# Kernel tuning notes

Measured on AMD Instinct MI355X. Metric: run time of the kernel, lower is better.

Reference implementation:

```python
import jax, jax.numpy as jnp
import numpy as np

B, S, E, H, L, OUT = 128, 256, 300, 512, 2, 2


def _lstm_dir(x, mask, w_ih, w_hh, b, h0, c0, reverse):
    """One direction of one LSTM layer with length masking (packed-seq semantics).
    x: [B,S,D], mask: [B,S] bool (t < length). Returns (outputs [B,S,H], final h [B,H]).
    For reverse=True, scan runs t=S-1..0; state only updates once t < length, which
    exactly reproduces pack_padded_sequence reverse-direction behavior.
    """
    def step(carry, inp):
        h, c = carry
        xt, mt = inp  # [B,D], [B]
        z = xt @ w_ih.T + h @ w_hh.T + b  # [B,4H], torch gate order i,f,g,o
        i, f, g, o = jnp.split(z, 4, axis=-1)
        c_new = jax.nn.sigmoid(f) * c + jax.nn.sigmoid(i) * jnp.tanh(g)
        h_new = jax.nn.sigmoid(o) * jnp.tanh(c_new)
        m = mt[:, None]
        h = jnp.where(m, h_new, h)
        c = jnp.where(m, c_new, c)
        return (h, c), h
    (hT, _), hs = jax.lax.scan(step, (h0, c0), (jnp.swapaxes(x, 0, 1), mask.T), reverse=reverse)
    return jnp.swapaxes(hs, 0, 1), hT


def setup_inputs():
    key = jax.random.key(0)
    ks = iter(jax.random.split(key, 32))
    lengths = jax.random.randint(next(ks), (B,), 1, S + 1)
    x = jax.random.normal(next(ks), (B, S, E), jnp.float32)
    # module encodes per-sample lengths in input[:, -1, 0]
    x = x.at[:, -1, 0].set(lengths.astype(jnp.float32))
    k = 1.0 / np.sqrt(H)
    def u(shape):
        return jax.random.uniform(next(ks), shape, jnp.float32, -k, k)
    d = {"x": x}
    for l in range(L):
        din = E if l == 0 else 2 * H
        for suf in ("f", "r"):
            d[f"w_ih_l{l}_{suf}"] = u((4 * H, din))
            d[f"w_hh_l{l}_{suf}"] = u((4 * H, H))
            d[f"b_ih_l{l}_{suf}"] = u((4 * H,))
            d[f"b_hh_l{l}_{suf}"] = u((4 * H,))
    d["fc1_w"] = u((H, H))
    d["fc1_b"] = u((H,))
    d["fc_w"] = u((OUT, H))
    d["fc_b"] = u((OUT,))
    return d


def _forward(x, params):
    Bx, Sx = x.shape[0], x.shape[1]
    lengths = jnp.minimum(x[:, -1, 0].astype(jnp.int32), Sx)  # clamp(max=seq_len)
    mask = jnp.arange(Sx)[None, :] < lengths[:, None]  # [B,S]
    h0 = jnp.ones((Bx, H), x.dtype)  # module uses ones, not zeros
    c0 = jnp.ones((Bx, H), x.dtype)
    inp = x
    hT_r = None
    for l in range(L):
        (wif, whf, bif, bhf), (wir, whr, bir, bhr) = params[l]
        out_f, _ = _lstm_dir(inp, mask, wif, whf, bif + bhf, h0, c0, False)
        out_r, hT_r = _lstm_dir(inp, mask, wir, whr, bir + bhr, h0, c0, True)
        inp = jnp.concatenate([out_f, out_r], axis=-1)  # [B,S,2H]
    # ht[-1] == final hidden of reverse direction of last layer
    return hT_r


def reference(x, w_ih_l0_f, w_hh_l0_f, b_ih_l0_f, b_hh_l0_f,
              w_ih_l0_r, w_hh_l0_r, b_ih_l0_r, b_hh_l0_r,
              w_ih_l1_f, w_hh_l1_f, b_ih_l1_f, b_hh_l1_f,
              w_ih_l1_r, w_hh_l1_r, b_ih_l1_r, b_hh_l1_r,
              fc1_w, fc1_b, fc_w, fc_b):
    params = [((w_ih_l0_f, w_hh_l0_f, b_ih_l0_f, b_hh_l0_f),
               (w_ih_l0_r, w_hh_l0_r, b_ih_l0_r, b_hh_l0_r)),
              ((w_ih_l1_f, w_hh_l1_f, b_ih_l1_f, b_hh_l1_f),
               (w_ih_l1_r, w_hh_l1_r, b_ih_l1_r, b_hh_l1_r))]
    ht = _forward(x, params)  # [B,H]
    out = ht @ fc1_w.T + fc1_b  # fc1 (no activation in original)
    return out @ fc_w.T + fc_b  # [B,OUT]
```

## Files before the change

### kernel.cpp

```cpp
#include <hip/hip_runtime.h>

#define B_  128
#define S_  256
#define E_  300
#define EP_ 320
#define H_  512
#define G_  2048
#define D1_ 1024

typedef _Float16 f16;
typedef __attribute__((ext_vector_type(8))) _Float16 f16x8;
typedef __attribute__((ext_vector_type(4))) float    f32x4;
typedef unsigned long long u64;
typedef unsigned int u32;

__device__ __forceinline__ float sigf(float x){ return 1.f/(1.f + __expf(-x)); }
__device__ __forceinline__ float tanhf_(float x){
  float e = __expf(-2.f*fabsf(x));
  float t = (1.f - e)/(1.f + e);
  return x < 0.f ? -t : t;
}

__device__ __forceinline__ u64 aload64(const u64* p){
  return __hip_atomic_load((u64*)p, __ATOMIC_RELAXED, __HIP_MEMORY_SCOPE_AGENT);
}
__device__ __forceinline__ void astore32(u32* p, u32 v){
  __hip_atomic_store(p, v, __ATOMIC_RELAXED, __HIP_MEMORY_SCOPE_AGENT);
}
union H8 { u64 q[2]; f16x8 v; };
union FU { f16 f; unsigned short s; };


__global__ void k_f32_to_f16(const float* __restrict__ s, f16* __restrict__ d, int n){
  int i = blockIdx.x*blockDim.x + threadIdx.x;
  if (i < n) d[i] = (f16)s[i];
}

__global__ void k_pad_w(const float* __restrict__ s, f16* __restrict__ d, int rows, int ks, int kd){
  int i = blockIdx.x*blockDim.x + threadIdx.x;
  if (i >= rows*kd) return;
  int r = i/kd, k = i - r*kd;
  d[i] = (k < ks) ? (f16)s[(size_t)r*ks + k] : (f16)0.f;
}

__global__ void k_bias(const float* __restrict__ a, const float* __restrict__ b,
                       float* __restrict__ d, int n){
  int i = blockIdx.x*blockDim.x + threadIdx.x;
  if (i < n) d[i] = a[i] + b[i];
}

__global__ void k_len(const float* __restrict__ x, int* __restrict__ len){
  int b = threadIdx.x;
  if (b < B_){
    int v = (int)x[((size_t)b*S_ + (S_-1))*E_];
    len[b] = v > S_ ? S_ : v;
  }
}

__global__ void k_init(f16* hxA, f16* hx1, float* cstate, u32* barA, u32* barC){
  int i = blockIdx.x*blockDim.x + threadIdx.x;
  if (i < B_*H_){
    hxA[i] = (f16)1.f;
    hxA[2*B_*H_ + i] = (f16)1.f;
    hx1[i] = (f16)1.f;
    cstate[i] = 1.f;
  }
  if (i < 4*S_) barA[i] = 0u;
  if (i < 2*S_) barC[i] = 0u;
}


__global__ __launch_bounds__(256) void k_gemm_bt(
    const f16* __restrict__ A, const f16* __restrict__ Bm,
    f16* __restrict__ C, const float* __restrict__ bias,
    int M, int N, int K)
{
  __shared__ f16 As[64*40];
  __shared__ f16 Bs[64*40];
  const int m0 = blockIdx.x*64, n0 = blockIdx.y*64;
  const int tid = threadIdx.x;
  const int w = tid>>6, lane = tid&63, quad = lane>>4, l16 = lane&15;
  const int wm = (w&1)*32, wn = (w>>1)*32;
  const int lr = tid>>2, lc = (tid&3)*8;
  const f16* Ap = A + (size_t)(m0+lr)*K + lc;
  const f16* Bp = Bm + (size_t)(n0+lr)*K + lc;
  f32x4 z4 = {0.f,0.f,0.f,0.f};
  f32x4 acc[2][2] = {{z4,z4},{z4,z4}};
  for (int k0 = 0; k0 < K; k0 += 32){
    *(uint4*)&As[lr*40+lc] = *(const uint4*)(Ap + k0);
    *(uint4*)&Bs[lr*40+lc] = *(const uint4*)(Bp + k0);
    __syncthreads();
    f16x8 a0 = *(const f16x8*)&As[(wm+l16)*40 + quad*8];
    f16x8 a1 = *(const f16x8*)&As[(wm+16+l16)*40 + quad*8];
    f16x8 b0 = *(const f16x8*)&Bs[(wn+l16)*40 + quad*8];
    f16x8 b1 = *(const f16x8*)&Bs[(wn+16+l16)*40 + quad*8];
    acc[0][0] = __builtin_amdgcn_mfma_f32_16x16x32_f16(a0,b0,acc[0][0],0,0,0);
    acc[0][1] = __builtin_amdgcn_mfma_f32_16x16x32_f16(a0,b1,acc[0][1],0,0,0);
    acc[1][0] = __builtin_amdgcn_mfma_f32_16x16x32_f16(a1,b0,acc[1][0],0,0,0);
    acc[1][1] = __builtin_amdgcn_mfma_f32_16x16x32_f16(a1,b1,acc[1][1],0,0,0);
    __syncthreads();
  }
#pragma unroll
  for (int mi = 0; mi < 2; ++mi)
#pragma unroll
    for (int ni = 0; ni < 2; ++ni){
      int col = n0 + wn + ni*16 + l16;
      float bz = bias[col];
#pragma unroll
      for (int r = 0; r < 4; ++r){
        int row = m0 + wm + mi*16 + quad*4 + r;
        C[(size_t)row*N + col] = (f16)(acc[mi][ni][r] + bz);
      }
    }
}


__global__ __launch_bounds__(256, 1) void k_phaseA(
    const float* __restrict__ x,
    const f16* __restrict__ w0f, const f16* __restrict__ w0r,
    const f16* __restrict__ whf, const f16* __restrict__ whr,
    const float* __restrict__ bs0, const int* __restrict__ len,
    f16* __restrict__ hxA, f16* __restrict__ outcat,
    u32* __restrict__ barA)
{
  __shared__ f16 Wh[64*512];
  __shared__ f16 Wi[64*320];
  const int half = blockIdx.x, jb = blockIdx.y, dir = blockIdx.z;
  const f16* wih = dir ? w0r : w0f;
  const f16* whh = dir ? whr : whf;
  const float* bias = bs0 + dir*G_;
  f16* hx = hxA + (size_t)dir*(2*B_*H_);
  u32* mybar = barA + (dir*2 + half)*S_;
  const int tid = threadIdx.x;
  const int w = tid>>6, lane = tid&63, quad = lane>>4, l16 = lane&15;
  const int j0 = jb*16;
  const int m0 = half*64 + w*16;

  for (int u = tid; u < 4096; u += 256){
    int lrr = u>>6, uc = u&63;
    int g = lrr>>4, i = lrr&15;
    *(uint4*)&Wh[lrr*512 + (uc ^ (i&7))*8] =
        *(const uint4*)(whh + ((size_t)(g*H_ + j0 + i))*H_ + uc*8);
  }
  for (int u = tid; u < 2560; u += 256){
    int row = u/40, c = u - row*40;
    int g = row>>4, i = row&15;
    *(uint4*)&Wi[row*320 + (c ^ (i&7))*8] =
        *(const uint4*)(wih + ((size_t)(g*H_ + j0 + i))*EP_ + c*8);
  }
  __syncthreads();

  const int j = j0 + l16;
  float bz[4], hprev[4], cpr[4]; int lm[4];
#pragma unroll
  for (int g = 0; g < 4; ++g) bz[g] = bias[g*H_ + j];
#pragma unroll
  for (int r = 0; r < 4; ++r){ hprev[r] = 1.f; cpr[r] = 1.f; lm[r] = len[m0 + quad*4 + r]; }
  const size_t xrowbase = (size_t)(m0 + l16)*S_;

  float4 xA[9], xB[9]; float xT[8];
  {
    const int t0 = dir ? (S_-1) : 0;
    const float* xr = x + (xrowbase + t0)*E_;
#pragma unroll
    for (int kb = 0; kb < 9; ++kb){
      xA[kb] = *(const float4*)(xr + kb*32 + quad*8);
      xB[kb] = *(const float4*)(xr + kb*32 + quad*8 + 4);
    }
    int kbase = 288 + quad*8;
#pragma unroll
    for (int e2 = 0; e2 < 8; ++e2)
      xT[e2] = (kbase + e2 < E_) ? xr[kbase + e2] : 0.f;
  }

  for (int s = 0; s < S_; ++s){
    const int t = dir ? (S_-1-s) : s;
    f32x4 z4 = {0.f,0.f,0.f,0.f};
    f32x4 acc[4] = {z4,z4,z4,z4};

#pragma unroll
    for (int kb = 0; kb < 9; ++kb){
      f16x8 a;
      a[0]=(f16)xA[kb].x; a[1]=(f16)xA[kb].y; a[2]=(f16)xA[kb].z; a[3]=(f16)xA[kb].w;
      a[4]=(f16)xB[kb].x; a[5]=(f16)xB[kb].y; a[6]=(f16)xB[kb].z; a[7]=(f16)xB[kb].w;
      int c = (kb*4 + quad) ^ (l16 & 7);
#pragma unroll
      for (int g = 0; g < 4; ++g){
        f16x8 b = *(const f16x8*)&Wi[(g*16+l16)*320 + c*8];
        acc[g] = __builtin_amdgcn_mfma_f32_16x16x32_f16(a, b, acc[g],0,0,0);
      }
    }
    {
      f16x8 a;
#pragma unroll
      for (int e2 = 0; e2 < 8; ++e2) a[e2] = (f16)xT[e2];
      int c = (36 + quad) ^ (l16 & 7);
#pragma unroll
      for (int g = 0; g < 4; ++g){
        f16x8 b = *(const f16x8*)&Wi[(g*16+l16)*320 + c*8];
        acc[g] = __builtin_amdgcn_mfma_f32_16x16x32_f16(a, b, acc[g],0,0,0);
      }
    }

    if (s+1 < S_){
      const int tn = dir ? (S_-2-s) : (s+1);
      const float* xr = x + (xrowbase + tn)*E_;
#pragma unroll
      for (int kb = 0; kb < 9; ++kb){
        xA[kb] = *(const float4*)(xr + kb*32 + quad*8);
        xB[kb] = *(const float4*)(xr + kb*32 + quad*8 + 4);
      }
      int kbase = 288 + quad*8;
#pragma unroll
      for (int e2 = 0; e2 < 8; ++e2)
        xT[e2] = (kbase + e2 < E_) ? xr[kbase + e2] : 0.f;
    }

    if (s > 0){
      while (__hip_atomic_load(&mybar[s-1], __ATOMIC_RELAXED, __HIP_MEMORY_SCOPE_AGENT) < 32u) {}
    }
    asm volatile("" ::: "memory");

    const int par = s & 1;
    const u64* hap = (const u64*)(hx + (size_t)par*(B_*H_) + (size_t)(m0 + l16)*H_);
    u64 hq[32];
#pragma unroll
    for (int kb = 0; kb < 16; ++kb){
      hq[2*kb]   = aload64(hap + kb*8 + quad*2);
      hq[2*kb+1] = aload64(hap + kb*8 + quad*2 + 1);
    }
#pragma unroll
    for (int kb = 0; kb < 16; ++kb){
      H8 ha;
      ha.q[0] = hq[2*kb];
      ha.q[1] = hq[2*kb+1];
      int uq = kb*4 + quad;
#pragma unroll
      for (int g = 0; g < 4; ++g){
        f16x8 b = *(const f16x8*)&Wh[(g*16+l16)*512 + ((uq ^ (l16&7)))*8];
        acc[g] = __builtin_amdgcn_mfma_f32_16x16x32_f16(ha.v, b, acc[g],0,0,0);
      }
    }

    f16* hn = hx + (size_t)(1-par)*(B_*H_);
#pragma unroll
    for (int r = 0; r < 4; ++r){
      int m = m0 + quad*4 + r;
      float zi = acc[0][r] + bz[0];
      float zf = acc[1][r] + bz[1];
      float zg = acc[2][r] + bz[2];
      float zo = acc[3][r] + bz[3];
      float ig = sigf(zi), fg = sigf(zf), gg = tanhf_(zg), og = sigf(zo);
      float cnew = fg*cpr[r] + ig*gg;
      float hnew = og*tanhf_(cnew);
      bool mk = t < lm[r];
      float hsel = mk ? hnew : hprev[r];
      cpr[r] = mk ? cnew : cpr[r];
      hprev[r] = hsel;
      FU cv; cv.f = (f16)hsel;
      int other = __shfl_down((int)cv.s, 1);
      if ((l16 & 1) == 0)
        astore32((u32*)(hn + (size_t)m*H_ + j), (u32)cv.s | ((u32)other << 16));
    }
    __syncthreads();
    if (tid == 0)
      __hip_atomic_fetch_add(&mybar[s], 1u, __ATOMIC_RELAXED, __HIP_MEMORY_SCOPE_AGENT);

#pragma unroll
    for (int r = 0; r < 4; ++r){
      int m = m0 + quad*4 + r;
      FU cv; cv.f = (f16)hprev[r];
      int other = __shfl_down((int)cv.s, 1);
      if ((l16 & 1) == 0)
        *(u32*)(outcat + ((size_t)t*B_ + m)*D1_ + dir*H_ + j) = (u32)cv.s | ((u32)other << 16);
    }
  }
}


__global__ __launch_bounds__(256, 1) void k_phaseCrec(
    const f16* __restrict__ Z1c, const f16* __restrict__ w1h,
    const int* __restrict__ len,
    f16* __restrict__ hx1, float* __restrict__ cstate, float* __restrict__ h1f,
    u32* __restrict__ barC, int s0, int CH)
{
  __shared__ f16 Wh[64*512];
  const int half = blockIdx.x, jb = blockIdx.y;
  u32* mybar = barC + half*S_;
  const int tid = threadIdx.x;
  const int w = tid>>6, lane = tid&63, quad = lane>>4, l16 = lane&15;
  const int j0 = jb*16;
  const int m0 = half*64 + w*16;

  for (int u = tid; u < 4096; u += 256){
    int lrr = u>>6, uc = u&63;
    int g = lrr>>4, i = lrr&15;
    *(uint4*)&Wh[lrr*512 + (uc ^ (i&7))*8] =
        *(const uint4*)(w1h + ((size_t)(g*H_ + j0 + i))*H_ + uc*8);
  }
  __syncthreads();

  const int j = j0 + l16;
  float hprev[4], cpr[4]; int lm[4];
#pragma unroll
  for (int r = 0; r < 4; ++r){
    int m = m0 + quad*4 + r;
    lm[r] = len[m];
    cpr[r] = cstate[(size_t)m*H_ + j];
    hprev[r] = (float)hx1[(size_t)(s0 & 1)*(B_*H_) + (size_t)m*H_ + j];
  }

  for (int sl = 0; sl < CH; ++sl){
    const int s = s0 + sl;
    const int t = S_-1-s;
    const int zrow = CH-1-sl;

    float zv[4][4];
#pragma unroll
    for (int g = 0; g < 4; ++g)
#pragma unroll
      for (int r = 0; r < 4; ++r)
        zv[g][r] = (float)Z1c[((size_t)zrow*B_ + m0 + quad*4 + r)*G_ + g*H_ + j];

    if (s > 0){
      while (__hip_atomic_load(&mybar[s-1], __ATOMIC_RELAXED, __HIP_MEMORY_SCOPE_AGENT) < 32u) {}
    }
    asm volatile("" ::: "memory");

    const int par = s & 1;
    const u64* hap = (const u64*)(hx1 + (size_t)par*(B_*H_) + (size_t)(m0 + l16)*H_);
    f32x4 z4 = {0.f,0.f,0.f,0.f};
    f32x4 acc[4] = {z4,z4,z4,z4};
    u64 hq[32];
#pragma unroll
    for (int kb = 0; kb < 16; ++kb){
      hq[2*kb]   = aload64(hap + kb*8 + quad*2);
      hq[2*kb+1] = aload64(hap + kb*8 + quad*2 + 1);
    }
#pragma unroll
    for (int kb = 0; kb < 16; ++kb){
      H8 ha;
      ha.q[0] = hq[2*kb];
      ha.q[1] = hq[2*kb+1];
      int uq = kb*4 + quad;
#pragma unroll
      for (int g = 0; g < 4; ++g){
        f16x8 b = *(const f16x8*)&Wh[(g*16+l16)*512 + ((uq ^ (l16&7)))*8];
        acc[g] = __builtin_amdgcn_mfma_f32_16x16x32_f16(ha.v, b, acc[g],0,0,0);
      }
    }

    f16* hn = hx1 + (size_t)(1-par)*(B_*H_);
#pragma unroll
    for (int r = 0; r < 4; ++r){
      int m = m0 + quad*4 + r;
      float zi = acc[0][r] + zv[0][r];
      float zf = acc[1][r] + zv[1][r];
      float zg = acc[2][r] + zv[2][r];
      float zo = acc[3][r] + zv[3][r];
      float ig = sigf(zi), fg = sigf(zf), gg = tanhf_(zg), og = sigf(zo);
      float cnew = fg*cpr[r] + ig*gg;
      float hnew = og*tanhf_(cnew);
      bool mk = t < lm[r];
      float hsel = mk ? hnew : hprev[r];
      cpr[r] = mk ? cnew : cpr[r];
      hprev[r] = hsel;
      FU cv; cv.f = (f16)hsel;
      int other = __shfl_down((int)cv.s, 1);
      if ((l16 & 1) == 0)
        astore32((u32*)(hn + (size_t)m*H_ + j), (u32)cv.s | ((u32)other << 16));
    }
    __syncthreads();
    if (tid == 0)
      __hip_atomic_fetch_add(&mybar[s], 1u, __ATOMIC_RELAXED, __HIP_MEMORY_SCOPE_AGENT);

    if (t == 0){
#pragma unroll
      for (int r = 0; r < 4; ++r)
        h1f[(size_t)(m0 + quad*4 + r)*H_ + j] = hprev[r];
    }
  }

#pragma unroll
  for (int r = 0; r < 4; ++r)
    cstate[(size_t)(m0 + quad*4 + r)*H_ + j] = cpr[r];
}


__global__ void k_fold(const float* __restrict__ fc1w, const float* __restrict__ fc1b,
                       const float* __restrict__ fcw,  const float* __restrict__ fcb,
                       float* __restrict__ Mf, float* __restrict__ bf){
  int i = blockIdx.x*blockDim.x + threadIdx.x;
  if (i >= 1024) return;
  int o = i >> 9, h = i & 511;
  float s = 0.f;
  for (int jj = 0; jj < 512; ++jj) s += fcw[o*512 + jj] * fc1w[jj*512 + h];
  Mf[o*512 + h] = s;
  if (h == 0){
    float sb = fcb[o];
    for (int jj = 0; jj < 512; ++jj) sb += fcw[o*512 + jj] * fc1b[jj];
    bf[o] = sb;
  }
}

__global__ void k_final(const float* __restrict__ h1f, const float* __restrict__ Mf,
                        const float* __restrict__ bf, float* __restrict__ out){
  int i = threadIdx.x;
  if (i >= 256) return;
  int b = i >> 1, o = i & 1;
  float s = bf[o];
  const float* hp = h1f + (size_t)b*512;
  const float* mp = Mf + (size_t)o*512;
  for (int h = 0; h < 512; ++h) s += hp[h]*mp[h];
  out[b*2 + o] = s;
}


extern "C" void kernel_launch(void* const* d_in, const int* in_sizes, int n_in,
                              void* d_out, int out_size, void* d_ws, size_t ws_size,
                              hipStream_t stream)
{
  const float* x     = (const float*)d_in[0];
  const float* wih0f = (const float*)d_in[1];
  const float* whh0f = (const float*)d_in[2];
  const float* bih0f = (const float*)d_in[3];
  const float* bhh0f = (const float*)d_in[4];
  const float* wih0r = (const float*)d_in[5];
  const float* whh0r = (const float*)d_in[6];
  const float* bih0r = (const float*)d_in[7];
  const float* bhh0r = (const float*)d_in[8];
  const float* wih1r = (const float*)d_in[13];
  const float* whh1r = (const float*)d_in[14];
  const float* bih1r = (const float*)d_in[15];
  const float* bhh1r = (const float*)d_in[16];
  const float* fc1w  = (const float*)d_in[17];
  const float* fc1b  = (const float*)d_in[18];
  const float* fcw   = (const float*)d_in[19];
  const float* fcb   = (const float*)d_in[20];
  float* out = (float*)d_out;

  char* p = (char*)d_ws;
  auto alloc = [&](size_t bytes)->char*{
    char* r = p; p += (bytes + 255) & ~(size_t)255; return r;
  };
  f16* w0fp   = (f16*)alloc((size_t)G_*EP_*2);
  f16* w0rp   = (f16*)alloc((size_t)G_*EP_*2);
  f16* whf    = (f16*)alloc((size_t)G_*H_*2);
  f16* whr    = (f16*)alloc((size_t)G_*H_*2);
  f16* w1i    = (f16*)alloc((size_t)G_*D1_*2);
  f16* w1h    = (f16*)alloc((size_t)G_*H_*2);
  float* bs0  = (float*)alloc((size_t)2*G_*4);
  float* bs1r = (float*)alloc(G_*4);
  int*   len  = (int*)alloc(B_*4);
  f16* outcat = (f16*)alloc((size_t)S_*B_*D1_*2);
  f16* hxA    = (f16*)alloc((size_t)2*2*B_*H_*2);
  f16* hx1    = (f16*)alloc((size_t)2*B_*H_*2);
  float* cstate=(float*)alloc((size_t)B_*H_*4);
  float* h1f  = (float*)alloc((size_t)B_*H_*4);
  float* Mf   = (float*)alloc(2*512*4);
  float* bf   = (float*)alloc(256);
  u32* barA   = (u32*)alloc(4*S_*4);
  u32* barC   = (u32*)alloc(2*S_*4);
  size_t used = (size_t)(p - (char*)d_ws);
  int CH = 8;
  for (int c = 256; c >= 8; c >>= 1){
    if (used + (size_t)c*B_*G_*2 <= ws_size){ CH = c; break; }
  }
  f16* Z1c = (f16*)alloc((size_t)CH*B_*G_*2);
  const int NC = S_/CH;

  int n;
  n = G_*EP_; k_pad_w<<<(n+255)/256, 256, 0, stream>>>(wih0f, w0fp, G_, E_, EP_);
              k_pad_w<<<(n+255)/256, 256, 0, stream>>>(wih0r, w0rp, G_, E_, EP_);
  n = G_*H_;  k_f32_to_f16<<<(n+255)/256,256,0,stream>>>(whh0f, whf, n);
              k_f32_to_f16<<<(n+255)/256,256,0,stream>>>(whh0r, whr, n);
              k_f32_to_f16<<<(n+255)/256,256,0,stream>>>(whh1r, w1h, n);
  n = G_*D1_; k_f32_to_f16<<<(n+255)/256,256,0,stream>>>(wih1r, w1i, n);
  k_bias<<<8,256,0,stream>>>(bih0f, bhh0f, bs0, G_);
  k_bias<<<8,256,0,stream>>>(bih0r, bhh0r, bs0 + G_, G_);
  k_bias<<<8,256,0,stream>>>(bih1r, bhh1r, bs1r, G_);
  k_len<<<1,128,0,stream>>>(x, len);
  k_init<<<(B_*H_+255)/256,256,0,stream>>>(hxA, hx1, cstate, barA, barC);
  k_fold<<<4,256,0,stream>>>(fc1w, fc1b, fcw, fcb, Mf, bf);

  k_phaseA<<<dim3(2,32,2), 256, 0, stream>>>(
      x, w0fp, w0rp, whf, whr, bs0, len, hxA, outcat, barA);

  for (int cc = 0; cc < NC; ++cc){
    int t0 = S_ - (cc+1)*CH;
    k_gemm_bt<<<dim3(CH*2,32), 256, 0, stream>>>(
        outcat + (size_t)t0*B_*D1_, w1i, Z1c, bs1r, CH*B_, G_, D1_);
    k_phaseCrec<<<dim3(2,32), 256, 0, stream>>>(
        Z1c, w1h, len, hx1, cstate, h1f, barC, cc*CH, CH);
  }

  k_final<<<1,256,0,stream>>>(h1f, Mf, bf, out);
}
```

Baseline: 4.277 ms.

## Replace block-wide atomic step barriers with per-wave flag slots in recurrent kernels

Both recurrent kernels previously ended each timestep with a __syncthreads plus a single-thread atomic increment on a shared per-step counter, and every block spun until the counter reached 32. Now each wave publishes its own flag, holding the step number, into a 4-slot ring once its stores have drained. Each consumer wave polls only the 32 producer flags for its own 16 rows, using a ballot. This removes the intra-block barrier and the contended atomic, so waves can proceed independently. In exchange it adds more polling traffic, and correctness depends on the double-buffered hidden state together with the step-valued flags ruling out reuse hazards.

```diff
diff --git a/kernel.cpp b/kernel.cpp
--- a/kernel.cpp
+++ b/kernel.cpp
@@ -7,6 +7,9 @@
 #define H_  512
 #define G_  2048
 #define D1_ 1024
+#define FSLOT_ 4
+#define FA_WORDS_ (4*FSLOT_*4*32*32)
+#define FC_WORDS_ (2*FSLOT_*4*32*32)
 
 typedef _Float16 f16;
 typedef __attribute__((ext_vector_type(8))) _Float16 f16x8;
@@ -24,6 +27,9 @@
 __device__ __forceinline__ u64 aload64(const u64* p){
   return __hip_atomic_load((u64*)p, __ATOMIC_RELAXED, __HIP_MEMORY_SCOPE_AGENT);
 }
+__device__ __forceinline__ u32 aload32(const u32* p){
+  return __hip_atomic_load((u32*)p, __ATOMIC_RELAXED, __HIP_MEMORY_SCOPE_AGENT);
+}
 __device__ __forceinline__ void astore32(u32* p, u32 v){
   __hip_atomic_store(p, v, __ATOMIC_RELAXED, __HIP_MEMORY_SCOPE_AGENT);
 }
@@ -57,7 +63,12 @@
   }
 }
 
-__global__ void k_init(f16* hxA, f16* hx1, float* cstate, u32* barA, u32* barC){
+__global__ void k_zero(u32* __restrict__ p, int n){
+  int i = blockIdx.x*blockDim.x + threadIdx.x;
+  if (i < n) p[i] = 0u;
+}
+
+__global__ void k_init(f16* hxA, f16* hx1, float* cstate){
   int i = blockIdx.x*blockDim.x + threadIdx.x;
   if (i < B_*H_){
     hxA[i] = (f16)1.f;
@@ -65,8 +76,6 @@
     hx1[i] = (f16)1.f;
     cstate[i] = 1.f;
   }
-  if (i < 4*S_) barA[i] = 0u;
-  if (i < 2*S_) barC[i] = 0u;
 }
 
 
@@ -121,7 +130,7 @@
     const f16* __restrict__ whf, const f16* __restrict__ whr,
     const float* __restrict__ bs0, const int* __restrict__ len,
     f16* __restrict__ hxA, f16* __restrict__ outcat,
-    u32* __restrict__ barA)
+    u32* __restrict__ flagsA)
 {
   __shared__ f16 Wh[64*512];
   __shared__ f16 Wi[64*320];
@@ -130,7 +139,7 @@
   const f16* whh = dir ? whr : whf;
   const float* bias = bs0 + dir*G_;
   f16* hx = hxA + (size_t)dir*(2*B_*H_);
-  u32* mybar = barA + (dir*2 + half)*S_;
+  u32* fbase = flagsA + (size_t)(dir*2 + half)*(FSLOT_*4*32*32);
   const int tid = threadIdx.x;
   const int w = tid>>6, lane = tid&63, quad = lane>>4, l16 = lane&15;
   const int j0 = jb*16;
@@ -217,9 +226,14 @@
     }
 
     if (s > 0){
-      while (__hip_atomic_load(&mybar[s-1], __ATOMIC_RELAXED, __HIP_MEMORY_SCOPE_AGENT) < 32u) {}
-    }
-    asm volatile("" ::: "memory");
+      const u32* fp = fbase + ((size_t)((s-1)&(FSLOT_-1))*4 + w)*32*32;
+      const u32 expv = (u32)s;
+      for (;;){
+        u32 v = aload32(fp + (size_t)(lane & 31)*32);
+        if (__ballot(v == expv) == ~0ull) break;
+      }
+      asm volatile("" ::: "memory");
+    }
 
     const int par = s & 1;
     const u64* hap = (const u64*)(hx + (size_t)par*(B_*H_) + (size_t)(m0 + l16)*H_);
@@ -262,9 +276,9 @@
       if ((l16 & 1) == 0)
         astore32((u32*)(hn + (size_t)m*H_ + j), (u32)cv.s | ((u32)other << 16));
     }
-    __syncthreads();
-    if (tid == 0)
-      __hip_atomic_fetch_add(&mybar[s], 1u, __ATOMIC_RELAXED, __HIP_MEMORY_SCOPE_AGENT);
+    asm volatile("s_waitcnt vmcnt(0)" ::: "memory");
+    if (lane == 0)
+      astore32(fbase + (((size_t)(s&(FSLOT_-1))*4 + w)*32 + jb)*32, (u32)(s+1));
 
 #pragma unroll
     for (int r = 0; r < 4; ++r){
@@ -282,11 +296,11 @@
     const f16* __restrict__ Z1c, const f16* __restrict__ w1h,
     const int* __restrict__ len,
     f16* __restrict__ hx1, float* __restrict__ cstate, float* __restrict__ h1f,
-    u32* __restrict__ barC, int s0, int CH)
+    u32* __restrict__ flagsC, int s0, int CH)
 {
   __shared__ f16 Wh[64*512];
   const int half = blockIdx.x, jb = blockIdx.y;
-  u32* mybar = barC + half*S_;
+  u32* fbase = flagsC + (size_t)half*(FSLOT_*4*32*32);
   const int tid = threadIdx.x;
   const int w = tid>>6, lane = tid&63, quad = lane>>4, l16 = lane&15;
   const int j0 = jb*16;
@@ -323,9 +337,14 @@
         zv[g][r] = (float)Z1c[((size_t)zrow*B_ + m0 + quad*4 + r)*G_ + g*H_ + j];
 
     if (s > 0){
-      while (__hip_atomic_load(&mybar[s-1], __ATOMIC_RELAXED, __HIP_MEMORY_SCOPE_AGENT) < 32u) {}
-    }
-    asm volatile("" ::: "memory");
+      const u32* fp = fbase + ((size_t)((s-1)&(FSLOT_-1))*4 + w)*32*32;
+      const u32 expv = (u32)s;
+      for (;;){
+        u32 v = aload32(fp + (size_t)(lane & 31)*32);
+        if (__ballot(v == expv) == ~0ull) break;
+      }
+      asm volatile("" ::: "memory");
+    }
 
     const int par = s & 1;
     const u64* hap = (const u64*)(hx1 + (size_t)par*(B_*H_) + (size_t)(m0 + l16)*H_);
@@ -370,9 +389,9 @@
       if ((l16 & 1) == 0)
         astore32((u32*)(hn + (size_t)m*H_ + j), (u32)cv.s | ((u32)other << 16));
     }
-    __syncthreads();
-    if (tid == 0)
-      __hip_atomic_fetch_add(&mybar[s], 1u, __ATOMIC_RELAXED, __HIP_MEMORY_SCOPE_AGENT);
+    asm volatile("s_waitcnt vmcnt(0)" ::: "memory");
+    if (lane == 0)
+      astore32(fbase + (((size_t)(s&(FSLOT_-1))*4 + w)*32 + jb)*32, (u32)(s+1));
 
     if (t == 0){
 #pragma unroll
@@ -459,8 +478,8 @@
   float* h1f  = (float*)alloc((size_t)B_*H_*4);
   float* Mf   = (float*)alloc(2*512*4);
   float* bf   = (float*)alloc(256);
-  u32* barA   = (u32*)alloc(4*S_*4);
-  u32* barC   = (u32*)alloc(2*S_*4);
+  u32* flagsA = (u32*)alloc((size_t)FA_WORDS_*4);
+  u32* flagsC = (u32*)alloc((size_t)FC_WORDS_*4);
   size_t used = (size_t)(p - (char*)d_ws);
   int CH = 8;
   for (int c = 256; c >= 8; c >>= 1){
@@ -480,18 +499,20 @@
   k_bias<<<8,256,0,stream>>>(bih0r, bhh0r, bs0 + G_, G_);
   k_bias<<<8,256,0,stream>>>(bih1r, bhh1r, bs1r, G_);
   k_len<<<1,128,0,stream>>>(x, len);
-  k_init<<<(B_*H_+255)/256,256,0,stream>>>(hxA, hx1, cstate, barA, barC);
+  k_init<<<(B_*H_+255)/256,256,0,stream>>>(hxA, hx1, cstate);
+  k_zero<<<(FA_WORDS_+255)/256,256,0,stream>>>(flagsA, FA_WORDS_);
+  k_zero<<<(FC_WORDS_+255)/256,256,0,stream>>>(flagsC, FC_WORDS_);
   k_fold<<<4,256,0,stream>>>(fc1w, fc1b, fcw, fcb, Mf, bf);
 
   k_phaseA<<<dim3(2,32,2), 256, 0, stream>>>(
-      x, w0fp, w0rp, whf, whr, bs0, len, hxA, outcat, barA);
+      x, w0fp, w0rp, whf, whr, bs0, len, hxA, outcat, flagsA);
 
   for (int cc = 0; cc < NC; ++cc){
     int t0 = S_ - (cc+1)*CH;
     k_gemm_bt<<<dim3(CH*2,32), 256, 0, stream>>>(
         outcat + (size_t)t0*B_*D1_, w1i, Z1c, bs1r, CH*B_, G_, D1_);
     k_phaseCrec<<<dim3(2,32), 256, 0, stream>>>(
-        Z1c, w1h, len, hx1, cstate, h1f, barC, cc*CH, CH);
+        Z1c, w1h, len, hx1, cstate, h1f, flagsC, cc*CH, CH);
   }
 
   k_final<<<1,256,0,stream>>>(h1f, Mf, bf, out);
```

Measured after the change: 4.108 ms. 4.0% less time.
